# Performance work log

Measured on AMD Instinct MI355X. Metric: run time of the kernel, lower is better.

## Reference

```python
import jax, jax.numpy as jnp
import numpy as np

B = 4096          # batch_size
D = 256           # embedding dim
N = 2 * B
TEMPERATURE = 0.5
GAMMA = 2.0
ALPHA = 0.25


def _negative_indices():
    # Static column indices of negatives per row: all columns except self (i)
    # and the positive partner ((i+B) mod N). Shape (N, N-2).
    idx = []
    for i in range(N):
        partner = (i + B) % N
        cols = [j for j in range(N) if j != i and j != partner]
        idx.append(cols)
    return np.asarray(idx, dtype=np.int32)

_NEG_IDX = jnp.asarray(_negative_indices())


def setup_inputs() -> dict:
    key = jax.random.key(0)
    kx, ky = jax.random.split(key)
    zx = jax.random.normal(kx, (B, D), dtype=jnp.float32)
    zy = jax.random.normal(ky, (B, D), dtype=jnp.float32)
    return {"zx": zx, "zy": zy}


def reference(zx, zy):
    z = jnp.concatenate([zx, zy], axis=0)                    # (N, D)
    zn = z / jnp.linalg.norm(z, axis=1, keepdims=True)       # cosine normalize
    sim = (zn @ zn.T) / TEMPERATURE                          # (N, N)

    sim_xy = jnp.diagonal(sim, offset=B)                     # (B,)
    sim_yx = jnp.diagonal(sim, offset=-B)                    # (B,)
    pos = jnp.concatenate([sim_xy, sim_yx])[:, None]         # (N, 1)
    neg = jnp.take_along_axis(sim, _NEG_IDX, axis=1)         # (N, N-2)

    logits = jnp.concatenate([pos, neg], axis=1)             # (N, N-1)
    # CE with label 0 for every row: -log_softmax(logits)[:, 0]
    ce = jax.nn.logsumexp(logits, axis=1) - logits[:, 0]
    pt = jnp.exp(-ce)
    focal = (1.0 - pt) ** GAMMA * ce
    return (ALPHA * focal).mean()
```

## Files before the change

kernel.cpp:

```cpp
#include <hip/hip_runtime.h>
#include <stdint.h>
#include <stddef.h>


typedef __attribute__((ext_vector_type(8))) short short8;
typedef __attribute__((ext_vector_type(4))) float f32x4;

#define NROWS 8192
#define DDIM 256
#define NTILES 2080
#define NBLK 512

__device__ __forceinline__ unsigned short f2bf(float f) {
  unsigned int u = __float_as_uint(f);
  u = (u + 0x7FFFu + ((u >> 16) & 1u)) >> 16;
  return (unsigned short)u;
}

__device__ __forceinline__ void unrank_tile(int t, int& p_out, int& q_out) {
  int p = (int)((129.0f - sqrtf((float)(16641 - 8 * t))) * 0.5f);
  p = max(0, min(63, p));
  while ((((p + 1) * (129 - (p + 1))) >> 1) <= t) ++p;
  while (((p * (129 - p)) >> 1) > t) --p;
  p_out = p;
  q_out = p + (t - ((p * (129 - p)) >> 1));
}

__global__ __launch_bounds__(256) void norm_kernel(const float* __restrict__ zx,
                                                   const float* __restrict__ zy,
                                                   unsigned short* __restrict__ zn,
                                                   unsigned int* __restrict__ counter) {
  if (blockIdx.x == 0 && threadIdx.x == 0) *counter = 0u;
  const int row = blockIdx.x * 4 + (threadIdx.x >> 6);
  const int lane = threadIdx.x & 63;
  const float* src = (row < 4096) ? (zx + (size_t)row * DDIM)
                                  : (zy + (size_t)(row - 4096) * DDIM);
  float4 v = reinterpret_cast<const float4*>(src)[lane];
  float ss = v.x * v.x + v.y * v.y + v.z * v.z + v.w * v.w;
#pragma unroll
  for (int m = 1; m < 64; m <<= 1) ss += __shfl_xor(ss, m);
  const float sc = 1.69864360f * rsqrtf(ss);
  ushort4 o;
  o.x = f2bf(v.x * sc); o.y = f2bf(v.y * sc);
  o.z = f2bf(v.z * sc); o.w = f2bf(v.w * sc);
  reinterpret_cast<ushort4*>(zn + (size_t)row * DDIM)[lane] = o;
}

__global__ __launch_bounds__(256, 2) void simtri_kernel(const unsigned short* __restrict__ zn,
                                                        float* __restrict__ partial,
                                                        float* __restrict__ pos) {
  __shared__ unsigned short smem[3][2][128 * 32];
  const int c = (blockIdx.x & 7) * 64 + (blockIdx.x >> 3);
  int start, nt;
  if (c < 32) { start = c * 5;              nt = 5; }
  else        { start = 160 + (c - 32) * 4; nt = 4; }
  const int NS = nt * 8;

  const int tid = threadIdx.x;
  const int lane = tid & 63;
  const int wid = tid >> 6;
  const int wr = wid >> 1;
  const int wc = wid & 1;
  const int hi = lane >> 4, lo = lane & 15;
  const int sw = lo & 3;

  const f32x4 z4 = {0.f, 0.f, 0.f, 0.f};
  f32x4 acc[4][4];
#pragma unroll
  for (int m = 0; m < 4; ++m)
#pragma unroll
    for (int n = 0; n < 4; ++n) acc[m][n] = z4;

  auto stage_pair = [&](int b, int p, int q, int k0) {
#pragma unroll
    for (int which = 0; which < 2; ++which) {
      const int row0 = (which ? q : p) << 7;
      unsigned short* lb = &smem[b][which][0];
#pragma unroll
      for (int j = 0; j < 2; ++j) {
        const int u = j * 256 + tid;
        const int r = u >> 2, ul = u & 3;
        const unsigned short* g =
            zn + (size_t)(row0 + r) * DDIM + k0 + ((ul ^ (r & 3)) << 3);
        unsigned short* l = lb + (size_t)(j * 256 + wid * 64) * 8;
        __builtin_amdgcn_global_load_lds(
            (const __attribute__((address_space(1))) void*)g,
            (__attribute__((address_space(3))) void*)l, 16, 0, 0);
      }
    }
  };

  auto consume = [&](int b) {
    const unsigned short* A = &smem[b][0][0];
    const unsigned short* Bm = &smem[b][1][0];
    short8 af[4], bfr[4];
#pragma unroll
    for (int m = 0; m < 4; ++m)
      af[m] = *reinterpret_cast<const short8*>(
          A + ((wr * 64 + m * 16 + lo) * 32 + ((hi ^ sw) << 3)));
#pragma unroll
    for (int n = 0; n < 4; ++n)
      bfr[n] = *reinterpret_cast<const short8*>(
          Bm + ((wc * 64 + n * 16 + lo) * 32 + ((hi ^ sw) << 3)));
#pragma unroll
    for (int m = 0; m < 4; ++m)
#pragma unroll
      for (int n = 0; n < 4; ++n)
        acc[m][n] = __builtin_amdgcn_mfma_f32_16x16x32_bf16(af[m], bfr[n], acc[m][n], 0, 0, 0);
  };

  auto advance = [&](int& p, int& q) {
    if (q == 63) { ++p; q = p; } else { ++q; }
  };

  auto epilogue = [&](int cp, int cq) {
    const bool isdiag = (cp == cq);
    const bool ispos = (cq == cp + 32);
    const int R0 = cp << 7;
    const int C0 = cq << 7;
    float rsum[4][4];
    float csum[4];
#pragma unroll
    for (int m = 0; m < 4; ++m)
#pragma unroll
      for (int r = 0; r < 4; ++r) rsum[m][r] = 0.f;
#pragma unroll
    for (int n = 0; n < 4; ++n) csum[n] = 0.f;
#pragma unroll
    for (int m = 0; m < 4; ++m)
#pragma unroll
      for (int n = 0; n < 4; ++n)
#pragma unroll
        for (int r = 0; r < 4; ++r) {
          const float e = __builtin_amdgcn_exp2f(acc[m][n][r]);
          rsum[m][r] += e;
          csum[n] += e;
        }
    if ((isdiag || ispos) && (wr == wc)) {
#pragma unroll
      for (int m = 0; m < 4; ++m)
#pragma unroll
        for (int r = 0; r < 4; ++r)
          if (lo == 4 * hi + r) {
            if (isdiag) rsum[m][r] -= __builtin_amdgcn_exp2f(acc[m][m][r]);
            else        pos[R0 + wr * 64 + m * 16 + lo] = acc[m][m][r];
          }
    }
#pragma unroll
    for (int m = 0; m < 4; ++m)
#pragma unroll
      for (int r = 0; r < 4; ++r) {
        float s = rsum[m][r];
        s += __shfl_xor(s, 1); s += __shfl_xor(s, 2);
        s += __shfl_xor(s, 4); s += __shfl_xor(s, 8);
        if (lo == 0) {
          const int grow = R0 + wr * 64 + m * 16 + (hi << 2) + r;
          partial[(size_t)(cq * 2 + wc) * NROWS + grow] = s;
        }
      }
    if (!isdiag) {
#pragma unroll
      for (int n = 0; n < 4; ++n) {
        float cs = csum[n];
        cs += __shfl_xor(cs, 16); cs += __shfl_xor(cs, 32);
        if (lane < 16)
          partial[(size_t)(cp * 2 + wr) * NROWS + (C0 + wc * 64 + n * 16 + lane)] = cs;
      }
    }
  };

  int cp, cq;
  unrank_tile(start, cp, cq);
  int sp = cp, sq = cq;
  stage_pair(0, sp, sq, 0);
  stage_pair(1, sp, sq, 32);
  stage_pair(2, sp, sq, 64);

  int bsel = 0;
  for (int k = 0; k < NS - 2; ++k) {
    asm volatile("s_waitcnt vmcnt(8)" ::: "memory");
    __builtin_amdgcn_s_barrier();
    __builtin_amdgcn_sched_barrier(0);
    consume(bsel);
    if ((k & 7) == 7) {
      epilogue(cp, cq);
      advance(cp, cq);
#pragma unroll
      for (int m = 0; m < 4; ++m)
#pragma unroll
        for (int n = 0; n < 4; ++n) acc[m][n] = z4;
    }
    __builtin_amdgcn_s_barrier();
    const int t = k + 3;
    if (t < NS) {
      if ((t & 7) == 0) advance(sp, sq);
      stage_pair(bsel, sp, sq, (t & 7) * 32);
    }
    bsel = (bsel == 2) ? 0 : bsel + 1;
  }
  asm volatile("s_waitcnt vmcnt(4)" ::: "memory");
  __builtin_amdgcn_s_barrier();
  __builtin_amdgcn_sched_barrier(0);
  consume(bsel);
  bsel = (bsel == 2) ? 0 : bsel + 1;
  asm volatile("s_waitcnt vmcnt(0)" ::: "memory");
  __builtin_amdgcn_s_barrier();
  __builtin_amdgcn_sched_barrier(0);
  consume(bsel);
  epilogue(cp, cq);
}

__global__ __launch_bounds__(256) void d1_kernel(const float* __restrict__ partial,
                                                 const float* __restrict__ pos,
                                                 float* __restrict__ bsum,
                                                 float* __restrict__ out,
                                                 unsigned int* __restrict__ counter) {
  const int row = blockIdx.x * 256 + threadIdx.x;
  float s = 0.f;
#pragma unroll 16
  for (int c = 0; c < 128; ++c) s += partial[(size_t)c * NROWS + row];
  const float L = __log2f(s) - pos[row & 4095];
  const float pt = __builtin_amdgcn_exp2f(-L);
  const float ce = 0.69314718056f * L;
  float f = (1.f - pt) * (1.f - pt) * ce;
#pragma unroll
  for (int m = 1; m < 64; m <<= 1) f += __shfl_xor(f, m);
  __shared__ float wsum[4];
  if ((threadIdx.x & 63) == 0) wsum[threadIdx.x >> 6] = f;
  __syncthreads();
  if (threadIdx.x == 0) {
    bsum[blockIdx.x] = wsum[0] + wsum[1] + wsum[2] + wsum[3];
    __threadfence();
    if (atomicAdd(counter, 1u) == 31u) {
      __threadfence();
      float v = 0.f;
#pragma unroll
      for (int c = 0; c < 32; ++c) v += ((const volatile float*)bsum)[c];
      out[0] = 0.25f * v / 8192.f;
    }
  }
}

extern "C" void kernel_launch(void* const* d_in, const int* in_sizes, int n_in,
                              void* d_out, int out_size, void* d_ws, size_t ws_size,
                              hipStream_t stream) {
  const float* zx = (const float*)d_in[0];
  const float* zy = (const float*)d_in[1];
  float* out = (float*)d_out;

  unsigned short* zn = (unsigned short*)d_ws;
  float* pos = (float*)((char*)d_ws + (size_t)NROWS * DDIM * 2);
  float* partial = pos + 4096;
  float* bsum = partial + (size_t)128 * NROWS;
  unsigned int* counter = (unsigned int*)(bsum + 32);

  norm_kernel<<<2048, 256, 0, stream>>>(zx, zy, zn, counter);
  simtri_kernel<<<NBLK, 256, 0, stream>>>(zn, partial, pos);
  d1_kernel<<<32, 256, 0, stream>>>(partial, pos, bsum, out, counter);
}
```

Before: 111.5 us.

## Deepen LDS pipeline to four stages, reorder tile schedule, defer partial stores

Moves the staging ring from three to four LDS buffers so that one more K-slice load is in flight before each consume. Replaces the triangular unranking with a per-XCD column-group tile ordering, aiming for better L2 locality on each XCD. Row and column partial sums now go to a shared-memory stash and are written to global memory together at the end of the block, so global stores leave the MFMA loop. The extra LDS (about 74 KB per block) may limit occupancy to two blocks per CU, and the new tile mapping has to cover every triangle tile exactly once.

```diff
diff --git a/kernel.cpp b/kernel.cpp
--- a/kernel.cpp
+++ b/kernel.cpp
@@ -8,22 +8,12 @@
 
 #define NROWS 8192
 #define DDIM 256
-#define NTILES 2080
 #define NBLK 512
 
 __device__ __forceinline__ unsigned short f2bf(float f) {
   unsigned int u = __float_as_uint(f);
   u = (u + 0x7FFFu + ((u >> 16) & 1u)) >> 16;
   return (unsigned short)u;
-}
-
-__device__ __forceinline__ void unrank_tile(int t, int& p_out, int& q_out) {
-  int p = (int)((129.0f - sqrtf((float)(16641 - 8 * t))) * 0.5f);
-  p = max(0, min(63, p));
-  while ((((p + 1) * (129 - (p + 1))) >> 1) <= t) ++p;
-  while (((p * (129 - p)) >> 1) > t) --p;
-  p_out = p;
-  q_out = p + (t - ((p * (129 - p)) >> 1));
 }
 
 __global__ __launch_bounds__(256) void norm_kernel(const float* __restrict__ zx,
@@ -49,12 +39,31 @@
 __global__ __launch_bounds__(256, 2) void simtri_kernel(const unsigned short* __restrict__ zn,
                                                         float* __restrict__ partial,
                                                         float* __restrict__ pos) {
-  __shared__ unsigned short smem[3][2][128 * 32];
-  const int c = (blockIdx.x & 7) * 64 + (blockIdx.x >> 3);
-  int start, nt;
-  if (c < 32) { start = c * 5;              nt = 5; }
-  else        { start = 160 + (c - 32) * 4; nt = 4; }
+  __shared__ unsigned short smem[4][2][128 * 32];
+  __shared__ float stash[5][4][128];
+  const int x = blockIdx.x & 7;
+  const int l = blockIdx.x >> 3;
+  int r0, nt;
+  if (l < 4) { r0 = l * 5;            nt = 5; }
+  else       { r0 = 20 + (l - 4) * 4; nt = 4; }
   const int NS = nt * 8;
+
+  auto advance = [&](int& p, int& q) {
+    if (p < q) { ++p; return; }
+    p = 0;
+    if ((q & 3) == 3) q = 4 * x; else ++q;
+  };
+  int cp = 0, cq = 4 * (15 - x);
+  {
+    int idx = r0;
+    while (true) {
+      const int len = cq + 1;
+      if (idx < len) { cp = idx; break; }
+      idx -= len;
+      if ((cq & 3) == 3) cq = 4 * x; else ++cq;
+    }
+  }
+  const int p0 = cp, q0 = cq;
 
   const int tid = threadIdx.x;
   const int lane = tid & 63;
@@ -109,15 +118,9 @@
         acc[m][n] = __builtin_amdgcn_mfma_f32_16x16x32_bf16(af[m], bfr[n], acc[m][n], 0, 0, 0);
   };
 
-  auto advance = [&](int& p, int& q) {
-    if (q == 63) { ++p; q = p; } else { ++q; }
-  };
-
-  auto epilogue = [&](int cp, int cq) {
-    const bool isdiag = (cp == cq);
-    const bool ispos = (cq == cp + 32);
-    const int R0 = cp << 7;
-    const int C0 = cq << 7;
+  auto epilogue = [&](int tp, int tq, int ti) {
+    const bool isdiag = (tp == tq);
+    const bool ispos = (tq == tp + 32);
     float rsum[4][4];
     float csum[4];
 #pragma unroll
@@ -143,7 +146,7 @@
         for (int r = 0; r < 4; ++r)
           if (lo == 4 * hi + r) {
             if (isdiag) rsum[m][r] -= __builtin_amdgcn_exp2f(acc[m][m][r]);
-            else        pos[R0 + wr * 64 + m * 16 + lo] = acc[m][m][r];
+            else        pos[(tp << 7) + wr * 64 + m * 16 + lo] = acc[m][m][r];
           }
     }
 #pragma unroll
@@ -153,37 +156,32 @@
         float s = rsum[m][r];
         s += __shfl_xor(s, 1); s += __shfl_xor(s, 2);
         s += __shfl_xor(s, 4); s += __shfl_xor(s, 8);
-        if (lo == 0) {
-          const int grow = R0 + wr * 64 + m * 16 + (hi << 2) + r;
-          partial[(size_t)(cq * 2 + wc) * NROWS + grow] = s;
-        }
+        if (lo == 0) stash[ti][wc][wr * 64 + m * 16 + (hi << 2) + r] = s;
       }
     if (!isdiag) {
 #pragma unroll
       for (int n = 0; n < 4; ++n) {
         float cs = csum[n];
         cs += __shfl_xor(cs, 16); cs += __shfl_xor(cs, 32);
-        if (lane < 16)
-          partial[(size_t)(cp * 2 + wr) * NROWS + (C0 + wc * 64 + n * 16 + lane)] = cs;
+        if (lane < 16) stash[ti][2 + wr][wc * 64 + n * 16 + lane] = cs;
       }
     }
   };
 
-  int cp, cq;
-  unrank_tile(start, cp, cq);
   int sp = cp, sq = cq;
   stage_pair(0, sp, sq, 0);
   stage_pair(1, sp, sq, 32);
   stage_pair(2, sp, sq, 64);
+  stage_pair(3, sp, sq, 96);
 
   int bsel = 0;
-  for (int k = 0; k < NS - 2; ++k) {
-    asm volatile("s_waitcnt vmcnt(8)" ::: "memory");
+  for (int k = 0; k < NS - 3; ++k) {
+    asm volatile("s_waitcnt vmcnt(12)" ::: "memory");
     __builtin_amdgcn_s_barrier();
     __builtin_amdgcn_sched_barrier(0);
     consume(bsel);
     if ((k & 7) == 7) {
-      epilogue(cp, cq);
+      epilogue(cp, cq, k >> 3);
       advance(cp, cq);
 #pragma unroll
       for (int m = 0; m < 4; ++m)
@@ -191,23 +189,39 @@
         for (int n = 0; n < 4; ++n) acc[m][n] = z4;
     }
     __builtin_amdgcn_s_barrier();
-    const int t = k + 3;
+    const int t = k + 4;
     if (t < NS) {
       if ((t & 7) == 0) advance(sp, sq);
       stage_pair(bsel, sp, sq, (t & 7) * 32);
     }
-    bsel = (bsel == 2) ? 0 : bsel + 1;
-  }
+    bsel = (bsel + 1) & 3;
+  }
+  asm volatile("s_waitcnt vmcnt(8)" ::: "memory");
+  __builtin_amdgcn_s_barrier();
+  __builtin_amdgcn_sched_barrier(0);
+  consume(bsel); bsel = (bsel + 1) & 3;
   asm volatile("s_waitcnt vmcnt(4)" ::: "memory");
   __builtin_amdgcn_s_barrier();
   __builtin_amdgcn_sched_barrier(0);
-  consume(bsel);
-  bsel = (bsel == 2) ? 0 : bsel + 1;
+  consume(bsel); bsel = (bsel + 1) & 3;
   asm volatile("s_waitcnt vmcnt(0)" ::: "memory");
   __builtin_amdgcn_s_barrier();
   __builtin_amdgcn_sched_barrier(0);
   consume(bsel);
-  epilogue(cp, cq);
+  epilogue(cp, cq, nt - 1);
+
+  __syncthreads();
+  {
+    int fp = p0, fq = q0;
+    const int half = tid >> 7;
+    const int rr = tid & 127;
+    for (int i = 0; i < nt; ++i) {
+      partial[(size_t)(fq * 2 + half) * NROWS + fp * 128 + rr] = stash[i][half][rr];
+      if (fp != fq)
+        partial[(size_t)(fp * 2 + half) * NROWS + fq * 128 + rr] = stash[i][2 + half][rr];
+      advance(fp, fq);
+    }
+  }
 }
 
 __global__ __launch_bounds__(256) void d1_kernel(const float* __restrict__ partial,
```

After: 113.6 us. About the same (+1.9%).
